# Kernel tuning notes

Measured on AMD Instinct MI355X. Metric: run time of the kernel, lower is better.

## Reference

```python
import jax, jax.numpy as jnp
import numpy as np

LEAK = 0.1  # LeakyReLU slope used throughout


def _conv(x, w, b, ph, pw):
    # NCHW conv, stride 1, asymmetric-free padding (ph on H, pw on W)
    y = jax.lax.conv_general_dilated(x, w, (1, 1), ((ph, ph), (pw, pw)),
                                     dimension_numbers=('NCHW', 'OIHW', 'NCHW'))
    return y + b[None, :, None, None]


def _pool2(x):
    B, C, H, W = x.shape
    return x.reshape(B, C, H // 2, 2, W // 2, 2).mean(axis=(3, 5))


def _lrelu(x):
    return jax.nn.leaky_relu(x, LEAK)


def _forward(x, label, g_style, spaced_style, char_style,
             sp1_w, sp2_w, in_w, in_b, c1w1, c1b1, c1w2, c1b2, c2w, c2b,
             c3w1, c3b1, c3w2, c3b2, fm_w, fm_b,
             cd_conv_w, cd_conv_b, cd_fc1_w, cd_fc1_b, cd_fc2_w, cd_fc2_b):
    B = x.shape[0]
    style1 = g_style @ sp1_w.T              # [B, dim//2]
    style2 = g_style @ sp2_w.T              # [B, dim]
    h = _lrelu(_conv(x, in_w, in_b, 0, 3))  # [B,dim,58,W]
    h = jnp.concatenate([h, jnp.broadcast_to(style1[:, :, None, None],
                        (B, style1.shape[1], h.shape[2], h.shape[3]))], axis=1)
    h = _lrelu(_conv(h, c1w1, c1b1, 0, 1))
    h = _pool2(h)
    m = _lrelu(_conv(h, c1w2, c1b2, 0, 1))  # [B,2dim,26,W/2]
    m2 = jnp.concatenate([m, jnp.broadcast_to(style2[:, :, None, None],
                         (B, style2.shape[1], m.shape[2], m.shape[3]))], axis=1)
    mL = _pool2(_lrelu(_conv(m2, c2w, c2b, 0, 1)))  # [B,2dim,12,W/4]
    lab = jnp.transpose(label, (1, 2, 0))           # [B, n_class, T]
    cls = jnp.argmax(lab, axis=1)                   # [B, T]
    hL, wL = mL.shape[2], mL.shape[3]
    lab_e = jnp.broadcast_to(lab[:, :, None, :], (B, lab.shape[1], hL, lab.shape[2]))
    sc = jnp.transpose(spaced_style, (1, 2, 0))     # [B, char_style_size, T]
    sc_e = jnp.broadcast_to(sc[:, :, None, :], (B, sc.shape[1], hL, sc.shape[2]))
    sal = jnp.concatenate([sc_e, lab_e], axis=1)[:, :, :, :wL]  # T == wL -> diff = 0
    mL = jnp.concatenate([mL, sal], axis=1)
    mL = _lrelu(_conv(mL, c3w1, c3b1, 0, 1))
    mL = _pool2(mL)
    mL = _lrelu(_conv(mL, c3w2, c3b2, 0, 1))        # [B, 4dim, 3, W/8]
    pM = _conv(mL, fm_w, fm_b, 0, 1)                # [B, 1, 1, W/8]
    # ---- per-character window gather + per-class expert dispatch ----
    T = label.shape[0]
    win = 2                                          # self.window
    mLp = jnp.pad(mL, ((0, 0), (0, 0), (0, 0), (win, win)))
    idx = jnp.arange(T) // 2                         # i = (i_orig + 0)//2 since diff==0
    cols = idx[:, None] + jnp.arange(2 * win + 1)    # [T,5] window cols in padded coords
    p = mLp[:, :, :, cols]                           # [B, 4dim, 3, T, 5]
    C4 = p.shape[1]
    p = jnp.transpose(p, (0, 3, 1, 2, 4)).reshape(B * T, C4, 3, 5)
    # CharDisc conv: 3x3 valid on [3,5] -> output 1x3; unfold the 3 windows
    wins = jnp.stack([p[..., w:w + 3] for w in range(3)], axis=1)  # [N,3,C4,3,3]
    pw = wins.reshape(B * T, 3, -1)                  # [N, 3, C4*9]
    cls_f = cls.reshape(-1)                          # [N] (all > 0 by construction)
    b_idx = jnp.repeat(jnp.arange(B), T)
    E = cd_conv_w.shape[0]
    Wsel = cd_conv_w.reshape(E, cd_conv_w.shape[1], -1)[cls_f]     # [N, 2dim, C4*9]
    co = jnp.einsum('nwd,nod->nwo', pw, Wsel) + cd_conv_b[cls_f][:, None, :]
    pooled = _lrelu(co).mean(axis=1)                 # conv -> LeakyReLU -> adaptive avg pool
    feat = jnp.concatenate([pooled, char_style[b_idx, cls_f]], axis=-1)  # [N, 2dim+cs]
    h1 = jax.nn.relu(jnp.einsum('nd,ndo->no', feat, cd_fc1_w[cls_f]) + cd_fc1_b[cls_f])
    pChar = jnp.einsum('nd,ndo->no', h1, cd_fc2_w[cls_f]) + cd_fc2_b[cls_f]  # [N,1]
    return pM, pChar


def setup_inputs():
    key = jax.random.key(0)
    ks = jax.random.split(key, 32)
    B, T, H, W = 2, 128, 64, 512
    NC, SS, CS, dim = 80, 256, 32, 64
    s = 0.05
    def rn(i, shape):
        return jax.random.normal(ks[i], shape, jnp.float32) * s
    cls_ids = jax.random.randint(ks[0], (T, B), 1, NC)  # class 0 = blank, never emitted
    return dict(
        x=jax.random.normal(ks[1], (B, 1, H, W), jnp.float32),
        label=jax.nn.one_hot(cls_ids, NC, dtype=jnp.float32),
        g_style=jax.random.normal(ks[2], (B, SS), jnp.float32),
        spaced_style=jax.random.normal(ks[3], (T, B, CS), jnp.float32),
        char_style=jax.random.normal(ks[4], (B, NC, CS), jnp.float32),
        sp1_w=rn(5, (dim // 2, SS)),
        sp2_w=rn(6, (dim, SS)),
        in_w=rn(7, (dim, 1, 7, 7)), in_b=rn(8, (dim,)),
        c1w1=rn(9, (dim, dim // 2 + dim, 3, 3)), c1b1=rn(10, (dim,)),
        c1w2=rn(11, (2 * dim, dim, 3, 3)), c1b2=rn(12, (2 * dim,)),
        c2w=rn(13, (2 * dim, dim + 2 * dim, 3, 3)), c2b=rn(14, (2 * dim,)),
        c3w1=rn(15, (2 * dim, NC + CS + 2 * dim, 3, 3)), c3b1=rn(16, (2 * dim,)),
        c3w2=rn(17, (4 * dim, 2 * dim, 3, 3)), c3b2=rn(18, (4 * dim,)),
        fm_w=rn(19, (1, 4 * dim, 3, 3)), fm_b=rn(20, (1,)),
        cd_conv_w=rn(21, (NC, 2 * dim, 4 * dim, 3, 3)), cd_conv_b=rn(22, (NC, 2 * dim)),
        cd_fc1_w=rn(23, (NC, 2 * dim + CS, 2 * dim)), cd_fc1_b=rn(24, (NC, 2 * dim)),
        cd_fc2_w=rn(25, (NC, 2 * dim, 1)), cd_fc2_b=rn(26, (NC, 1)),
    )


def reference(x, label, g_style, spaced_style, char_style,
              sp1_w, sp2_w, in_w, in_b, c1w1, c1b1, c1w2, c1b2, c2w, c2b,
              c3w1, c3b1, c3w2, c3b2, fm_w, fm_b,
              cd_conv_w, cd_conv_b, cd_fc1_w, cd_fc1_b, cd_fc2_w, cd_fc2_b):
    return _forward(x, label, g_style, spaced_style, char_style,
                    sp1_w, sp2_w, in_w, in_b, c1w1, c1b1, c1w2, c1b2, c2w, c2b,
                    c3w1, c3b1, c3w2, c3b2, fm_w, fm_b,
                    cd_conv_w, cd_conv_b, cd_fc1_w, cd_fc1_b, cd_fc2_w, cd_fc2_b)
```

## Files before the change

### kernel.cpp

```cpp
#include <hip/hip_runtime.h>
#include <hip/hip_bf16.h>

#define LEAKC 0.1f

__device__ __forceinline__ float lrelu(float v){ return v > 0.f ? v : LEAKC*v; }
__device__ __forceinline__ ushort f2b(float f){
  __hip_bfloat16 h = __float2bfloat16(f);
  return *reinterpret_cast<ushort*>(&h);
}
__device__ __forceinline__ float b2f(ushort u){
  __hip_bfloat16 h = *reinterpret_cast<__hip_bfloat16*>(&u);
  return __bfloat162float(h);
}

typedef __attribute__((ext_vector_type(8))) short bf16x8;
typedef __attribute__((ext_vector_type(4))) float f32x4;
typedef __attribute__((ext_vector_type(8))) unsigned short ushort8;

__device__ __forceinline__ void pack1(int idx, const float* __restrict__ w,
                                      ushort* __restrict__ wb, int CM, int CTOT){
  int c = idx % CM; int r = idx / CM; int t = r % 9; int n = r / 9;
  wb[idx] = f2b(w[((size_t)n*CTOT + c)*9 + t]);
}

__global__ __launch_bounds__(256) void prep_kernel(
    const float* __restrict__ g, const float* __restrict__ sp1, const float* __restrict__ sp2,
    const float* __restrict__ c1w1, const float* __restrict__ c1b1,
    const float* __restrict__ c1w2,
    const float* __restrict__ c2w,  const float* __restrict__ c2b,
    const float* __restrict__ c3w1, const float* __restrict__ c3b1,
    const float* __restrict__ c3w2,
    const float* __restrict__ label, const float* __restrict__ spaced,
    const float* __restrict__ x, const float* __restrict__ in_w, const float* __restrict__ in_b,
    float* __restrict__ map1, float* __restrict__ map2, float* __restrict__ map6,
    int* __restrict__ clsb, int* __restrict__ cnt, int* __restrict__ off, int* __restrict__ order,
    ushort* __restrict__ Wb2, ushort* __restrict__ Wb4, ushort* __restrict__ Wb5,
    ushort* __restrict__ Wb6, ushort* __restrict__ Wb7,
    ushort* __restrict__ h1b){
  int t = threadIdx.x;
  int bid = blockIdx.x;
  if (bid == 0){
    __shared__ float s1s[64], s2s[128];
    if (t < 64){
      int b = t >> 5, j = t & 31;
      float a = 0.f;
      for (int k=0;k<256;k++) a += g[b*256+k]*sp1[j*256+k];
      s1s[t] = a;
    } else if (t < 192){
      int u = t - 64;
      int b = u >> 6, j = u & 63;
      float a = 0.f;
      for (int k=0;k<256;k++) a += g[b*256+k]*sp2[j*256+k];
      s2s[u] = a;
    }
    __syncthreads();
    if (t < 128){
      int b = t >> 6, o = t & 63;
      float S0=0.f,S1=0.f,S2=0.f;
      for (int c=0;c<32;c++){
        float s = s1s[b*32+c];
        const float* wq = c1w1 + ((size_t)o*96 + 64 + c)*9;
        S0 += s*(wq[0]+wq[3]+wq[6]);
        S1 += s*(wq[1]+wq[4]+wq[7]);
        S2 += s*(wq[2]+wq[5]+wq[8]);
      }
      float bb = c1b1[o];
      map1[t*3+0]=S1+S2+bb; map1[t*3+1]=S0+S1+S2+bb; map1[t*3+2]=S0+S1+bb;
    }
    {
      int b = t >> 7, o = t & 127;
      float S0=0.f,S1=0.f,S2=0.f;
      for (int c=0;c<64;c++){
        float s = s2s[b*64+c];
        const float* wq = c2w + ((size_t)o*192 + 128 + c)*9;
        S0 += s*(wq[0]+wq[3]+wq[6]);
        S1 += s*(wq[1]+wq[4]+wq[7]);
        S2 += s*(wq[2]+wq[5]+wq[8]);
      }
      float bb = c2b[o];
      map2[t*3+0]=S1+S2+bb; map2[t*3+1]=S0+S1+S2+bb; map2[t*3+2]=S0+S1+bb;
    }
  } else if (bid == 1){
    __shared__ int h[80], hoff[80];
    if (t < 80) h[t] = 0;
    __syncthreads();
    int b = t >> 7, tt = t & 127;
    const float* p = label + (tt*2 + b)*80;
    float best = p[0]; int bi = 0;
    for (int c=1;c<80;c++){ float v = p[c]; if (v > best){ best = v; bi = c; } }
    clsb[t] = bi;
    atomicAdd(&h[bi], 1);
    __syncthreads();
    if (t == 0){
      int s = 0;
      for (int e=0;e<80;e++){ hoff[e] = s; s += h[e]; }
    }
    __syncthreads();
    if (t < 80){ cnt[t] = h[t]; off[t] = hoff[t]; }
    __syncthreads();
    int rank = atomicAdd(&hoff[bi], 1);
    order[rank] = t;
  } else if (bid < 130){
    int n = (bid - 2)*256 + t;
    int w = n & 127, o = (n >> 7) & 127, b = n >> 14;
    float a = c3b1[o];
    #pragma unroll
    for (int tt=0;tt<3;tt++){
      int j = w + tt - 1;
      if (j < 0 || j >= 128) continue;
      const float* sp = spaced + (j*2 + b)*32;
      const float* lb = label + (j*2 + b)*80;
      for (int c=0;c<32;c++){
        const float* wq = c3w1 + ((size_t)o*240 + 128 + c)*9 + tt;
        a += sp[c]*(wq[0]+wq[3]+wq[6]);
      }
      for (int c=0;c<80;c++){
        const float* wq = c3w1 + ((size_t)o*240 + 160 + c)*9 + tt;
        a += lb[c]*(wq[0]+wq[3]+wq[6]);
      }
    }
    map6[n] = a;
  } else if (bid < 2866){
    int i = (bid - 130)*256 + t;
    if      (i < 36864)  pack1(i,        c1w1, Wb2, 64, 96);
    else if (i < 110592) pack1(i-36864,  c1w2, Wb4, 64, 64);
    else if (i < 258048) pack1(i-110592, c2w,  Wb5, 128, 192);
    else if (i < 405504) pack1(i-258048, c3w1, Wb6, 128, 240);
    else if (i < 700416) pack1(i-405504, c3w2, Wb7, 128, 128);
  } else {
    int bid2 = bid - 2866;
    int xb = bid2 % 116;
    int og = (bid2 / 116) & 7;
    int b  = bid2 / (116*8);
    int hw = xb*256 + t;
    int y = hw >> 9, w = hw & 511;
    int o0 = og * 8;
    float acc[8];
    #pragma unroll
    for (int i=0;i<8;i++) acc[i] = in_b[o0+i];
    for (int kh=0;kh<7;kh++){
      const float* ip = x + ((size_t)b*64 + y + kh)*512;
      #pragma unroll
      for (int kw=0;kw<7;kw++){
        int wi = w + kw - 3;
        float v = (wi>=0 && wi<512) ? ip[wi] : 0.f;
        #pragma unroll
        for (int i=0;i<8;i++) acc[i] += v * in_w[(o0+i)*49 + kh*7 + kw];
      }
    }
    #pragma unroll
    for (int i=0;i<8;i++)
      h1b[((size_t)(b*64 + o0+i)*58 + y)*512 + w] = f2b(lrelu(acc[i]));
  }
}

template<int CM,int WID,int HIN,int COUT,int MODE,int OUTBF,int POOLIN>
__global__ __launch_bounds__(256) void conv_mfma(
    const ushort* __restrict__ in,
    const ushort* __restrict__ Wb,
    const float*  __restrict__ mb,
    float* __restrict__ outf,
    ushort* __restrict__ outh){
  constexpr int HOUT = HIN - 2;
  constexpr int KTOT = CM*9;
  constexpr int SLABS = CM/32;
  constexpr int NST = 3*SLABS;
  constexpr int HINF = 2*HIN;
  constexpr int WIDF = 2*WID;
  __shared__ ushort A[2][66][40];
  int tid = threadIdx.x, lane = tid & 63, wave = tid >> 6;
  int mt = blockIdx.x;
  int y  = mt / (WID/64), w0 = (mt % (WID/64))*64;
  int n0 = blockIdx.y*64;
  int b  = blockIdx.z;

  f32x4 acc[4];
  #pragma unroll
  for (int nf=0;nf<4;nf++) acc[nf] = (f32x4){0.f,0.f,0.f,0.f};

  auto stage = [&](int s, int bufi){
    int kh = s / SLABS;
    int c0s = (s % SLABS)*32;
    int c2 = (tid & 15)*2, m0v = (tid >> 4)*4;
    uint* dst = (uint*)&A[bufi][1+m0v][c2];
    if (POOLIN){
      const ushort* q0 = in + ((size_t)(b*CM + c0s + c2)*HINF + 2*(y+kh))*WIDF + 2*(w0 + m0v);
      const ushort* q1 = q0 + (size_t)HINF*WIDF;
      ushort8 a0 = *(const ushort8*)q0;
      ushort8 a1 = *(const ushort8*)(q0 + WIDF);
      ushort8 b0 = *(const ushort8*)q1;
      ushort8 b1 = *(const ushort8*)(q1 + WIDF);
      #pragma unroll
      for (int k=0;k<4;k++){
        float pa = 0.25f*(b2f(a0[2*k])+b2f(a0[2*k+1])+b2f(a1[2*k])+b2f(a1[2*k+1]));
        float pb = 0.25f*(b2f(b0[2*k])+b2f(b0[2*k+1])+b2f(b1[2*k])+b2f(b1[2*k+1]));
        dst[k*20] = (uint)f2b(pa) | ((uint)f2b(pb) << 16);
      }
      if (tid < 64){
        int c = tid & 31, side = tid >> 5;
        int wp = side ? (w0 + 64) : (w0 - 1);
        ushort v = 0;
        if (wp >= 0 && wp < WID){
          const ushort* q = in + ((size_t)(b*CM + c0s + c)*HINF + 2*(y+kh))*WIDF + 2*wp;
          v = f2b(0.25f*(b2f(q[0])+b2f(q[1])+b2f(q[WIDF])+b2f(q[WIDF+1])));
        }
        A[bufi][side ? 65 : 0][c] = v;
      }
    } else {
      const ushort* base = in + ((size_t)(b*CM + c0s)*HIN + (y+kh))*WID;
      const ushort* p0 = base + (size_t)c2*HIN*WID + w0 + m0v;
      const ushort* p1 = p0 + (size_t)HIN*WID;
      ushort4 va = *(const ushort4*)p0;
      ushort4 vb = *(const ushort4*)p1;
      dst[0]  = (uint)va.x | ((uint)vb.x << 16);
      dst[20] = (uint)va.y | ((uint)vb.y << 16);
      dst[40] = (uint)va.z | ((uint)vb.z << 16);
      dst[60] = (uint)va.w | ((uint)vb.w << 16);
      if (tid < 64){
        int c = tid & 31, side = tid >> 5;
        int w = side ? (w0 + 64) : (w0 - 1);
        ushort v = 0;
        if (w >= 0 && w < WID) v = base[(size_t)c*HIN*WID + w];
        A[bufi][side ? 65 : 0][c] = v;
      }
    }
  };

  stage(0, 0);
  __syncthreads();
  for (int s = 0; s < NST; ++s){
    int cur = s & 1;
    if (s + 1 < NST) stage(s+1, cur ^ 1);
    int kh = s / SLABS;
    int c0 = (s % SLABS)*32;
    #pragma unroll
    for (int kw = 0; kw < 3; ++kw){
      bf16x8 a = *(bf16x8*)&A[cur][wave*16 + (lane & 15) + kw][(lane >> 4)*8];
      #pragma unroll
      for (int nf = 0; nf < 4; ++nf){
        const ushort* wp = Wb + (size_t)(n0 + nf*16 + (lane & 15))*KTOT
                              + (kh*3 + kw)*CM + c0 + (lane >> 4)*8;
        bf16x8 bb = *(const bf16x8*)wp;
        acc[nf] = __builtin_amdgcn_mfma_f32_16x16x32_bf16(a, bb, acc[nf], 0, 0, 0);
      }
    }
    __syncthreads();
  }

  int mrow = wave*16 + ((lane >> 4) << 2);
  int w = w0 + mrow;
  #pragma unroll
  for (int nf = 0; nf < 4; ++nf){
    int n = n0 + nf*16 + (lane & 15);
    float r0 = acc[nf][0], r1 = acc[nf][1], r2 = acc[nf][2], r3 = acc[nf][3];
    if (MODE == 0){
      float bb = mb[n];
      r0 += bb; r1 += bb; r2 += bb; r3 += bb;
    } else if (MODE == 1){
      const float* m3 = mb + (size_t)(b*COUT + n)*3;
      float mL = m3[0], mM = m3[1], mR = m3[2];
      r0 += (w == 0) ? mL : ((w   == WID-1) ? mR : mM);
      r1 += (w+1 == WID-1) ? mR : mM;
      r2 += (w+2 == WID-1) ? mR : mM;
      r3 += (w+3 == WID-1) ? mR : mM;
    } else {
      const float* m6 = mb + ((size_t)(b*COUT + n))*WID + w;
      r0 += m6[0]; r1 += m6[1]; r2 += m6[2]; r3 += m6[3];
    }
    r0 = lrelu(r0); r1 = lrelu(r1); r2 = lrelu(r2); r3 = lrelu(r3);
    size_t off = ((size_t)(b*COUT + n)*HOUT + y)*WID + w;
    if (OUTBF){
      ushort4 o = make_ushort4(f2b(r0), f2b(r1), f2b(r2), f2b(r3));
      *(ushort4*)(outh + off) = o;
    } else {
      *(float4*)(outf + off) = make_float4(r0, r1, r2, r3);
    }
  }
}

__global__ __launch_bounds__(256) void fmim_kernel(const float* __restrict__ A7,
                          const float* __restrict__ fw,
                          const float* __restrict__ fb,
                          float* __restrict__ out,
                          ushort* __restrict__ pwgh){
  if (blockIdx.x < 128){
    __shared__ float red[4];
    int n = blockIdx.x;
    int b = n >> 6, w = n & 63;
    int c = threadIdx.x;
    float a = 0.f;
    #pragma unroll
    for (int r=0;r<3;r++){
      const float* ip = A7 + ((b*256+c)*3+r)*64;
      const float* wp = fw + (c*3+r)*3;
      #pragma unroll
      for (int kw=0;kw<3;kw++){
        int wi = w + kw - 1;
        if (wi>=0 && wi<64) a += ip[wi]*wp[kw];
      }
    }
    #pragma unroll
    for (int off=32; off>0; off>>=1) a += __shfl_down(a, off, 64);
    if ((threadIdx.x & 63) == 0) red[threadIdx.x>>6] = a;
    __syncthreads();
    if (threadIdx.x == 0) out[n] = red[0]+red[1]+red[2]+red[3] + fb[0];
  } else {
    int i = (blockIdx.x - 128)*256 + threadIdx.x;
    if (i >= 256*3*2304) return;
    int d = i % 2304; int rj = i / 2304; int j = rj % 3; int n = rj / 3;
    int b = n >> 7, t = n & 127; int idx = t >> 1;
    int c = d / 9, rem = d - c*9, r = rem / 3, kw = rem - r*3;
    int col = idx - 2 + kw + j;
    pwgh[i] = (col >= 0 && col < 64) ? f2b(A7[((size_t)(b*256 + c)*3 + r)*64 + col]) : (ushort)0;
  }
}

__global__ __launch_bounds__(256) void cd_conv_kernel(
    const ushort* __restrict__ pwgh,
    const int*   __restrict__ cnt,
    const int*   __restrict__ offv,
    const int*   __restrict__ order,
    const float* __restrict__ Wc,
    float* __restrict__ comat)
{
  __shared__ int rowOff[48];
  __shared__ f32x4 red[4][3][64];
  int e = blockIdx.x, og = blockIdx.y;
  int m = cnt[e];
  if (m == 0) return;
  int base = offv[e];
  int tid = threadIdx.x, lane = tid & 63, wave = tid >> 6;

  const float* wb_base = Wc + ((size_t)(e*128) + og*16 + (lane & 15))*2304;
  int kbase = wave*576 + ((lane >> 4)*8);

  for (int s0 = 0; s0 < m; s0 += 16){
    int rowsChunk = 3*(m - s0); if (rowsChunk > 48) rowsChunk = 48;
    if (tid < 48){
      int lr = s0 + tid/3;
      rowOff[tid] = (lr < m) ? (order[base+lr]*3 + (tid - (tid/3)*3))*2304 : -1;
    }
    __syncthreads();

    int offA[3];
    #pragma unroll
    for (int mt=0; mt<3; mt++) offA[mt] = rowOff[mt*16 + (lane & 15)];

    f32x4 acc[3];
    #pragma unroll
    for (int mt=0; mt<3; mt++) acc[mt] = (f32x4){0.f,0.f,0.f,0.f};

    for (int kk = 0; kk < 18; ++kk){
      int k0 = kbase + kk*32;
      const float* wb = wb_base + k0;
      float4 wv0 = *(const float4*)wb;
      float4 wv1 = *(const float4*)(wb + 4);
      bf16x8 bfr = { (short)f2b(wv0.x), (short)f2b(wv0.y), (short)f2b(wv0.z), (short)f2b(wv0.w),
                     (short)f2b(wv1.x), (short)f2b(wv1.y), (short)f2b(wv1.z), (short)f2b(wv1.w) };
      #pragma unroll
      for (int mt=0; mt<3; mt++){
        if (mt*16 < rowsChunk){
          bf16x8 af = {0,0,0,0,0,0,0,0};
          if (offA[mt] >= 0) af = *(const bf16x8*)&pwgh[offA[mt] + k0];
          acc[mt] = __builtin_amdgcn_mfma_f32_16x16x32_bf16(af, bfr, acc[mt], 0, 0, 0);
        }
      }
    }

    #pragma unroll
    for (int mt=0; mt<3; mt++) red[wave][mt][lane] = acc[mt];
    __syncthreads();

    if (wave < 3){
      int mt = wave;
      if (mt*16 < rowsChunk){
        f32x4 s4 = red[0][mt][lane];
        #pragma unroll
        for (int w2=1; w2<4; w2++){
          f32x4 t4 = red[w2][mt][lane];
          s4[0]+=t4[0]; s4[1]+=t4[1]; s4[2]+=t4[2]; s4[3]+=t4[3];
        }
        int col = og*16 + (lane & 15);
        #pragma unroll
        for (int r=0; r<4; r++){
          int row = mt*16 + ((lane >> 4) << 2) + r;
          if (row < rowsChunk){
            int lrank = s0 + row/3, j = row - (row/3)*3;
            int n = order[base + lrank];
            comat[((size_t)n*128 + col)*3 + j] = s4[r];
          }
        }
      }
    }
    __syncthreads();
  }
}

__global__ __launch_bounds__(128) void cd_tail_kernel(
    const float* __restrict__ comat,
    const int*   __restrict__ clsb,
    const float* __restrict__ bcv,
    const float* __restrict__ cstyle,
    const float* __restrict__ W1,
    const float* __restrict__ b1,
    const float* __restrict__ W2,
    const float* __restrict__ b2,
    float* __restrict__ pChar)
{
  __shared__ float feat[160];
  __shared__ float red2[2];
  int n = blockIdx.x, tid = threadIdx.x;
  int b = n >> 7;
  int e = clsb[n];
  int o = tid;
  const float* cm = comat + ((size_t)n*128 + o)*3;
  float bb = bcv[e*128 + o];
  feat[o] = (lrelu(cm[0]+bb) + lrelu(cm[1]+bb) + lrelu(cm[2]+bb)) * (1.f/3.f);
  if (tid < 32) feat[128+tid] = cstyle[(b*80 + e)*32 + tid];
  __syncthreads();

  float s = b1[e*128 + o];
  for (int d=0;d<160;d++) s += feat[d]*W1[(e*160 + d)*128 + o];
  float h = s > 0.f ? s : 0.f;
  float contrib = h * W2[e*128 + o];
  #pragma unroll
  for (int off=32; off>0; off>>=1) contrib += __shfl_down(contrib, off, 64);
  if ((tid & 63) == 0) red2[tid>>6] = contrib;
  __syncthreads();
  if (tid == 0) pChar[n] = red2[0] + red2[1] + b2[e];
}

extern "C" void kernel_launch(void* const* d_in, const int* in_sizes, int n_in,
                              void* d_out, int out_size, void* d_ws, size_t ws_size,
                              hipStream_t stream){
  (void)in_sizes; (void)n_in; (void)out_size; (void)ws_size;
  const float* x      = (const float*)d_in[0];
  const float* label  = (const float*)d_in[1];
  const float* g_style= (const float*)d_in[2];
  const float* spaced = (const float*)d_in[3];
  const float* cstyle = (const float*)d_in[4];
  const float* sp1    = (const float*)d_in[5];
  const float* sp2    = (const float*)d_in[6];
  const float* in_w   = (const float*)d_in[7];
  const float* in_b   = (const float*)d_in[8];
  const float* c1w1   = (const float*)d_in[9];
  const float* c1b1   = (const float*)d_in[10];
  const float* c1w2   = (const float*)d_in[11];
  const float* c1b2   = (const float*)d_in[12];
  const float* c2w    = (const float*)d_in[13];
  const float* c2b    = (const float*)d_in[14];
  const float* c3w1   = (const float*)d_in[15];
  const float* c3b1   = (const float*)d_in[16];
  const float* c3w2   = (const float*)d_in[17];
  const float* c3b2   = (const float*)d_in[18];
  const float* fm_w   = (const float*)d_in[19];
  const float* fm_b   = (const float*)d_in[20];
  const float* cdw    = (const float*)d_in[21];
  const float* cdb    = (const float*)d_in[22];
  const float* fc1w   = (const float*)d_in[23];
  const float* fc1b   = (const float*)d_in[24];
  const float* fc2w   = (const float*)d_in[25];
  const float* fc2b   = (const float*)d_in[26];
  float* out = (float*)d_out;
  char* ws = (char*)d_ws;

  ushort* h1b  = (ushort*)(ws + 0);
  ushort* A2h  = (ushort*)(ws + 7602176);
  ushort* pwgh = (ushort*)(ws + 14942208);
  ushort* A4b  = (ushort*)(ws + 18481152);
  ushort* A5h  = (ushort*)(ws + 21889024);
  ushort* A6b  = (ushort*)(ws + 25034752);
  float*  A7   = (float*) (ws + 25690112);
  float*  comat= (float*) (ws + 27262976);
  ushort* Wb2  = (ushort*)(ws + 27656192);
  ushort* Wb4  = (ushort*)(ws + 27729920);
  ushort* Wb5  = (ushort*)(ws + 27877376);
  ushort* Wb6  = (ushort*)(ws + 28172288);
  ushort* Wb7  = (ushort*)(ws + 28467200);
  float*  map6 = (float*) (ws + 29057024);
  float*  map1 = (float*) (ws + 29188096);
  float*  map2 = (float*) (ws + 29189632);
  int*    clsb = (int*)   (ws + 29192704);
  int*    order= (int*)   (ws + 29193728);
  int*    cntv = (int*)   (ws + 29194752);
  int*    offv = (int*)   (ws + 29195072);

  prep_kernel<<<4722,256,0,stream>>>(g_style, sp1, sp2, c1w1, c1b1, c1w2, c2w, c2b,
                                     c3w1, c3b1, c3w2, label, spaced,
                                     x, in_w, in_b,
                                     map1, map2, map6, clsb, cntv, offv, order,
                                     Wb2, Wb4, Wb5, Wb6, Wb7, h1b);

  conv_mfma<64,512,58,64,1,1,0><<<dim3(448,1,2),256,0,stream>>>(h1b, Wb2, map1, nullptr, A2h);
  conv_mfma<64,256,28,128,0,1,1><<<dim3(104,2,2),256,0,stream>>>(A2h, Wb4, c1b2, nullptr, A4b);
  conv_mfma<128,256,26,128,1,1,0><<<dim3(96,2,2),256,0,stream>>>(A4b, Wb5, map2, nullptr, A5h);
  conv_mfma<128,128,12,128,2,1,1><<<dim3(20,2,2),256,0,stream>>>(A5h, Wb6, map6, nullptr, A6b);
  conv_mfma<128,64,5,256,0,0,1><<<dim3(3,4,2),256,0,stream>>>(A6b, Wb7, c3b2, A7, nullptr);
  fmim_kernel<<<7040,256,0,stream>>>(A7, fm_w, fm_b, out, pwgh);
  cd_conv_kernel<<<dim3(80,8),256,0,stream>>>(pwgh, cntv, offv, order, cdw, comat);
  cd_tail_kernel<<<256,128,0,stream>>>(comat, clsb, cdb, cstyle, fc1w, fc1b, fc2w, fc2b, out + 128);
}
```

Baseline: 249.4 us.

## Defer map6 and late-layer weight packing into first conv kernel's extra blocks

Takes the map6 label/style contribution and the bf16 packing of the c2w, c3w1 and c3w2 weights out of the prep kernel. That work now runs in extra auxiliary blocks appended to the grid of the first MFMA conv launch. The aim is to shorten the prep kernel and let this independent work overlap with the first convolution's compute. The cost is a larger grid for the first conv, and every conv instantiation now takes extra pointer arguments.

```diff
diff --git a/kernel.cpp b/kernel.cpp
--- a/kernel.cpp
+++ b/kernel.cpp
@@ -28,14 +28,11 @@
     const float* __restrict__ c1w1, const float* __restrict__ c1b1,
     const float* __restrict__ c1w2,
     const float* __restrict__ c2w,  const float* __restrict__ c2b,
-    const float* __restrict__ c3w1, const float* __restrict__ c3b1,
-    const float* __restrict__ c3w2,
-    const float* __restrict__ label, const float* __restrict__ spaced,
+    const float* __restrict__ label,
     const float* __restrict__ x, const float* __restrict__ in_w, const float* __restrict__ in_b,
-    float* __restrict__ map1, float* __restrict__ map2, float* __restrict__ map6,
+    float* __restrict__ map1, float* __restrict__ map2,
     int* __restrict__ clsb, int* __restrict__ cnt, int* __restrict__ off, int* __restrict__ order,
-    ushort* __restrict__ Wb2, ushort* __restrict__ Wb4, ushort* __restrict__ Wb5,
-    ushort* __restrict__ Wb6, ushort* __restrict__ Wb7,
+    ushort* __restrict__ Wb2, ushort* __restrict__ Wb4,
     ushort* __restrict__ h1b){
   int t = threadIdx.x;
   int bid = blockIdx.x;
@@ -100,35 +97,12 @@
     __syncthreads();
     int rank = atomicAdd(&hoff[bi], 1);
     order[rank] = t;
-  } else if (bid < 130){
-    int n = (bid - 2)*256 + t;
-    int w = n & 127, o = (n >> 7) & 127, b = n >> 14;
-    float a = c3b1[o];
-    #pragma unroll
-    for (int tt=0;tt<3;tt++){
-      int j = w + tt - 1;
-      if (j < 0 || j >= 128) continue;
-      const float* sp = spaced + (j*2 + b)*32;
-      const float* lb = label + (j*2 + b)*80;
-      for (int c=0;c<32;c++){
-        const float* wq = c3w1 + ((size_t)o*240 + 128 + c)*9 + tt;
-        a += sp[c]*(wq[0]+wq[3]+wq[6]);
-      }
-      for (int c=0;c<80;c++){
-        const float* wq = c3w1 + ((size_t)o*240 + 160 + c)*9 + tt;
-        a += lb[c]*(wq[0]+wq[3]+wq[6]);
-      }
-    }
-    map6[n] = a;
-  } else if (bid < 2866){
-    int i = (bid - 130)*256 + t;
-    if      (i < 36864)  pack1(i,        c1w1, Wb2, 64, 96);
-    else if (i < 110592) pack1(i-36864,  c1w2, Wb4, 64, 64);
-    else if (i < 258048) pack1(i-110592, c2w,  Wb5, 128, 192);
-    else if (i < 405504) pack1(i-258048, c3w1, Wb6, 128, 240);
-    else if (i < 700416) pack1(i-405504, c3w2, Wb7, 128, 128);
+  } else if (bid < 434){
+    int i = (bid - 2)*256 + t;
+    if (i < 36864) pack1(i, c1w1, Wb2, 64, 96);
+    else           pack1(i-36864, c1w2, Wb4, 64, 64);
   } else {
-    int bid2 = bid - 2866;
+    int bid2 = bid - 434;
     int xb = bid2 % 116;
     int og = (bid2 / 116) & 7;
     int b  = bid2 / (116*8);
@@ -154,13 +128,49 @@
   }
 }
 
-template<int CM,int WID,int HIN,int COUT,int MODE,int OUTBF,int POOLIN>
+template<int CM,int WID,int HIN,int COUT,int MODE,int OUTBF,int POOLIN,int AUX>
 __global__ __launch_bounds__(256) void conv_mfma(
     const ushort* __restrict__ in,
     const ushort* __restrict__ Wb,
     const float*  __restrict__ mb,
     float* __restrict__ outf,
-    ushort* __restrict__ outh){
+    ushort* __restrict__ outh,
+    const float* __restrict__ c2w_,  const float* __restrict__ c3w1_,
+    const float* __restrict__ c3w2_, const float* __restrict__ label_,
+    const float* __restrict__ spaced_, const float* __restrict__ c3b1_,
+    ushort* __restrict__ Wb5_, ushort* __restrict__ Wb6_, ushort* __restrict__ Wb7_,
+    float* __restrict__ map6_){
+  if (AUX > 0 && (int)blockIdx.x >= AUX){
+    int aux_id = ((int)blockIdx.x - AUX)*2 + (int)blockIdx.z;
+    int t = threadIdx.x;
+    if (aux_id < 128){
+      int n = aux_id*256 + t;
+      int w = n & 127, o = (n >> 7) & 127, b = n >> 14;
+      float a = c3b1_[o];
+      #pragma unroll
+      for (int tt=0;tt<3;tt++){
+        int j = w + tt - 1;
+        if (j < 0 || j >= 128) continue;
+        const float* sp = spaced_ + (j*2 + b)*32;
+        const float* lb = label_ + (j*2 + b)*80;
+        for (int c=0;c<32;c++){
+          const float* wq = c3w1_ + ((size_t)o*240 + 128 + c)*9 + tt;
+          a += sp[c]*(wq[0]+wq[3]+wq[6]);
+        }
+        for (int c=0;c<80;c++){
+          const float* wq = c3w1_ + ((size_t)o*240 + 160 + c)*9 + tt;
+          a += lb[c]*(wq[0]+wq[3]+wq[6]);
+        }
+      }
+      map6_[n] = a;
+    } else {
+      int i = (aux_id - 128)*256 + t + 110592;
+      if      (i < 258048) pack1(i-110592, c2w_,  Wb5_, 128, 192);
+      else if (i < 405504) pack1(i-258048, c3w1_, Wb6_, 128, 240);
+      else if (i < 700416) pack1(i-405504, c3w2_, Wb7_, 128, 128);
+    }
+    return;
+  }
   constexpr int HOUT = HIN - 2;
   constexpr int KTOT = CM*9;
   constexpr int SLABS = CM/32;
@@ -485,17 +495,26 @@
   int*    cntv = (int*)   (ws + 29194752);
   int*    offv = (int*)   (ws + 29195072);
 
-  prep_kernel<<<4722,256,0,stream>>>(g_style, sp1, sp2, c1w1, c1b1, c1w2, c2w, c2b,
-                                     c3w1, c3b1, c3w2, label, spaced,
-                                     x, in_w, in_b,
-                                     map1, map2, map6, clsb, cntv, offv, order,
-                                     Wb2, Wb4, Wb5, Wb6, Wb7, h1b);
-
-  conv_mfma<64,512,58,64,1,1,0><<<dim3(448,1,2),256,0,stream>>>(h1b, Wb2, map1, nullptr, A2h);
-  conv_mfma<64,256,28,128,0,1,1><<<dim3(104,2,2),256,0,stream>>>(A2h, Wb4, c1b2, nullptr, A4b);
-  conv_mfma<128,256,26,128,1,1,0><<<dim3(96,2,2),256,0,stream>>>(A4b, Wb5, map2, nullptr, A5h);
-  conv_mfma<128,128,12,128,2,1,1><<<dim3(20,2,2),256,0,stream>>>(A5h, Wb6, map6, nullptr, A6b);
-  conv_mfma<128,64,5,256,0,0,1><<<dim3(3,4,2),256,0,stream>>>(A6b, Wb7, c3b2, A7, nullptr);
+  prep_kernel<<<2290,256,0,stream>>>(g_style, sp1, sp2, c1w1, c1b1, c1w2, c2w, c2b,
+                                     label, x, in_w, in_b,
+                                     map1, map2, clsb, cntv, offv, order,
+                                     Wb2, Wb4, h1b);
+
+  conv_mfma<64,512,58,64,1,1,0,448><<<dim3(448+1216,1,2),256,0,stream>>>(
+      h1b, Wb2, map1, nullptr, A2h,
+      c2w, c3w1, c3w2, label, spaced, c3b1, Wb5, Wb6, Wb7, map6);
+  conv_mfma<64,256,28,128,0,1,1,0><<<dim3(104,2,2),256,0,stream>>>(
+      A2h, Wb4, c1b2, nullptr, A4b,
+      c2w, c3w1, c3w2, label, spaced, c3b1, Wb5, Wb6, Wb7, map6);
+  conv_mfma<128,256,26,128,1,1,0,0><<<dim3(96,2,2),256,0,stream>>>(
+      A4b, Wb5, map2, nullptr, A5h,
+      c2w, c3w1, c3w2, label, spaced, c3b1, Wb5, Wb6, Wb7, map6);
+  conv_mfma<128,128,12,128,2,1,1,0><<<dim3(20,2,2),256,0,stream>>>(
+      A5h, Wb6, map6, nullptr, A6b,
+      c2w, c3w1, c3w2, label, spaced, c3b1, Wb5, Wb6, Wb7, map6);
+  conv_mfma<128,64,5,256,0,0,1,0><<<dim3(3,4,2),256,0,stream>>>(
+      A6b, Wb7, c3b2, A7, nullptr,
+      c2w, c3w1, c3w2, label, spaced, c3b1, Wb5, Wb6, Wb7, map6);
   fmim_kernel<<<7040,256,0,stream>>>(A7, fm_w, fm_b, out, pwgh);
   cd_conv_kernel<<<dim3(80,8),256,0,stream>>>(pwgh, cntv, offv, order, cdw, comat);
   cd_tail_kernel<<<256,128,0,stream>>>(comat, clsb, cdb, cstyle, fc1w, fc1b, fc2w, fc2b, out + 128);
```

Result: slower. 284.0 us (+13.9%).
